# Kernel optimization log

Measured on AMD Instinct MI355X. Metric: run time of the kernel, lower is better.

The kernel has to match this reference:

```python
import jax, jax.numpy as jnp
import numpy as np

N = 1_000_000          # total nodes across the batch of graphs
B = 4096               # number of graphs
EMB = 64               # embed_dim * heads = 32 * 2
FUSED = 3 * EMB        # 192


def _gelu(x):
    # torch nn.GELU default = exact (erf) form
    return jax.nn.gelu(x, approximate=False)


def setup_inputs() -> dict:
    key = jax.random.key(0)
    ks = jax.random.split(key, 30)
    s = 0.02
    inp = {
        "x_ped": jax.random.normal(ks[0], (N, 2), jnp.float32),
        "x_hazard": jax.random.normal(ks[1], (N, 3), jnp.float32),
        "x_infra": jax.random.normal(ks[2], (N, 3), jnp.float32),
        "batch": jnp.sort(jax.random.randint(ks[3], (N,), 0, B)),
        "num_graphs": B,
        # _MLPBranch params: Linear(d, 64) -> GELU -> Linear(64, 64)
        "ped_W1": jax.random.normal(ks[4], (2, EMB), jnp.float32) * s,
        "ped_b1": jnp.zeros((EMB,), jnp.float32),
        "ped_W2": jax.random.normal(ks[5], (EMB, EMB), jnp.float32) * s,
        "ped_b2": jnp.zeros((EMB,), jnp.float32),
        "haz_W1": jax.random.normal(ks[6], (3, EMB), jnp.float32) * s,
        "haz_b1": jnp.zeros((EMB,), jnp.float32),
        "haz_W2": jax.random.normal(ks[7], (EMB, EMB), jnp.float32) * s,
        "haz_b2": jnp.zeros((EMB,), jnp.float32),
        "inf_W1": jax.random.normal(ks[8], (3, EMB), jnp.float32) * s,
        "inf_b1": jnp.zeros((EMB,), jnp.float32),
        "inf_W2": jax.random.normal(ks[9], (EMB, EMB), jnp.float32) * s,
        "inf_b2": jnp.zeros((EMB,), jnp.float32),
        # dense heads
        "fc1_W": jax.random.normal(ks[10], (FUSED, 256), jnp.float32) * s,
        "fc1_b": jnp.zeros((256,), jnp.float32),
        "fc2_W": jax.random.normal(ks[11], (256, 128), jnp.float32) * s,
        "fc2_b": jnp.zeros((128,), jnp.float32),
        "sh_W": jax.random.normal(ks[12], (128, 1), jnp.float32) * s,
        "sh_b": jnp.zeros((1,), jnp.float32),
        "gd_W": jax.random.normal(ks[13], (128, 1), jnp.float32) * s,
        "gd_b": jnp.zeros((1,), jnp.float32),
        # critic: 192 -> 128 -> 64 -> 1 with GELU between
        "c1_W": jax.random.normal(ks[14], (FUSED, 128), jnp.float32) * s,
        "c1_b": jnp.zeros((128,), jnp.float32),
        "c2_W": jax.random.normal(ks[15], (128, 64), jnp.float32) * s,
        "c2_b": jnp.zeros((64,), jnp.float32),
        "c3_W": jax.random.normal(ks[16], (64, 1), jnp.float32) * s,
        "c3_b": jnp.zeros((1,), jnp.float32),
    }
    return inp


def _branch(x, W1, b1, W2, b2):
    # _MLPBranch: Linear -> GELU -> Linear
    return _gelu(x @ W1 + b1) @ W2 + b2


def reference(x_ped, x_hazard, x_infra, batch, num_graphs,
              ped_W1, ped_b1, ped_W2, ped_b2,
              haz_W1, haz_b1, haz_W2, haz_b2,
              inf_W1, inf_b1, inf_W2, inf_b2,
              fc1_W, fc1_b, fc2_W, fc2_b,
              sh_W, sh_b, gd_W, gd_b,
              c1_W, c1_b, c2_W, c2_b, c3_W, c3_b):
    ped_emb = _gelu(_branch(x_ped, ped_W1, ped_b1, ped_W2, ped_b2))
    haz_emb = _gelu(_branch(x_hazard, haz_W1, haz_b1, haz_W2, haz_b2))
    inf_emb = _gelu(_branch(x_infra, inf_W1, inf_b1, inf_W2, inf_b2))
    node_feat = jnp.concatenate([ped_emb, haz_emb, inf_emb], axis=-1)  # (N, 192)

    # per-graph masked mean pooling -> fused segment mean (empty graphs -> zeros)
    seg_sum = jax.ops.segment_sum(node_feat, batch, num_segments=num_graphs)  # (B, 192)
    counts = jax.ops.segment_sum(jnp.ones((node_feat.shape[0],), node_feat.dtype),
                                 batch, num_segments=num_graphs)
    graph_embed = seg_sum / jnp.maximum(counts, 1.0)[:, None]

    dense = _gelu(graph_embed @ fc1_W + fc1_b)
    dense = _gelu(dense @ fc2_W + fc2_b)
    shelter_logits = dense @ sh_W + sh_b
    guidance_logits = dense @ gd_W + gd_b

    v = _gelu(graph_embed @ c1_W + c1_b)
    v = _gelu(v @ c2_W + c2_b)
    value = (v @ c3_W + c3_b).squeeze(-1)
    return shelter_logits, guidance_logits, value
```

## Files before the change

kernel.cpp:

```cpp
#include <hip/hip_runtime.h>
#include <hip/hip_bf16.h>
#include <math.h>

#define EMB 64
#define NFEAT 192

typedef __attribute__((ext_vector_type(8))) short bf16x8;
typedef __attribute__((ext_vector_type(4))) float f32x4;

__device__ __forceinline__ float gelu_n(float x) {
    float y = x * x;
    float G = fmaf(y, fmaf(y, 9.97355701e-3f, -6.64903800e-2f), 3.98942280e-1f);
    return fmaf(0.5f, x, y * G);
}
__device__ __forceinline__ float gelu_head(float x) {
    float y = x * x;
    float G = fmaf(y, fmaf(y, fmaf(y, fmaf(y, 1.15434688e-4f, -1.18732821e-3f),
                                   9.97355701e-3f), -6.64903800e-2f), 3.98942280e-1f);
    float r = fmaf(0.5f, x, y * G);
    if (__builtin_expect(__any(y > 0.25f), 0))
        r = 0.5f * x * (1.0f + erff(x * 0.70710678118654752f));
    return r;
}

__device__ __forceinline__ unsigned short f32_bf16(float f) {
    unsigned u = __float_as_uint(f);
    u = (u + 0x7FFFu + ((u >> 16) & 1u)) >> 16;
    return (unsigned short)u;
}
__device__ __forceinline__ float bf16_f32(unsigned short h) {
    return __uint_as_float(((unsigned)h) << 16);
}

__global__ __launch_bounds__(256) void prep_pack(
    const float* __restrict__ pW2, const float* __restrict__ hW2,
    const float* __restrict__ iW2,
    unsigned short* __restrict__ whi, unsigned short* __restrict__ wlo,
    float4* __restrict__ zbase, int nzero4)
{
    int t = blockIdx.x * blockDim.x + threadIdx.x;
    if (t < nzero4) {
        float4 z = {0.f, 0.f, 0.f, 0.f};
        zbase[t] = z;
    }
    if (t >= 3 * 4096) return;
    int br = t >> 12, r = t & 4095;
    int k = r >> 6, j = r & 63;
    const float* src = br == 0 ? pW2 : (br == 1 ? hW2 : iW2);
    float w = src[k * 64 + j];
    unsigned short hi = f32_bf16(w);
    unsigned short lo = f32_bf16(w - bf16_f32(hi));
    int ks = k >> 5, lgrp = (k >> 3) & 3, i = k & 7;
    int nt = j >> 4, col = j & 15;
    int f = (ks * 4 + nt) * 64 + lgrp * 16 + col;
    whi[br * 4096 + f * 8 + i] = hi;
    wlo[br * 4096 + f * 8 + i] = lo;
}

template <int D>
__device__ __forceinline__ void do_branch(
    const float* __restrict__ xsrc, int n0,
    const float* __restrict__ W1, const float* __restrict__ b1,
    const float* __restrict__ b2,
    const unsigned short* __restrict__ whi, const unsigned short* __restrict__ wlo,
    int lane, int g, int g0, int g63, bool uniform,
    float* __restrict__ seg, float* __restrict__ seg_lane, int boff)
{
    const int lg = lane >> 4, lc = lane & 15;

    float xs[4][3];
#pragma unroll
    for (int m = 0; m < 4; m++) {
        int nm = n0 + m * 16 + lc;
        if (D == 2) {
            float2 t = ((const float2*)xsrc)[nm];
            xs[m][0] = t.x; xs[m][1] = t.y; xs[m][2] = 0.f;
        } else {
            xs[m][0] = xsrc[3 * nm + 0];
            xs[m][1] = xsrc[3 * nm + 1];
            xs[m][2] = xsrc[3 * nm + 2];
        }
    }

    const float* __restrict__ W1p = W1 + lg * 8;
    const float* __restrict__ b1p = b1 + lg * 8;
    const float* __restrict__ b2p = b2 + lc;
    const char*  __restrict__ WHp = (const char*)whi + lane * 16;
    const char*  __restrict__ WLp = (const char*)wlo + lane * 16;

    union AF { bf16x8 v; unsigned u[4]; };
    AF af[4][2];
#pragma unroll
    for (int ks = 0; ks < 2; ks++) {
        float w1r[D][8];
#pragma unroll
        for (int d = 0; d < D; d++) {
            float4 a = *(const float4*)(W1p + ks * 32 + d * EMB);
            float4 b = *(const float4*)(W1p + ks * 32 + d * EMB + 4);
            w1r[d][0] = a.x; w1r[d][1] = a.y; w1r[d][2] = a.z; w1r[d][3] = a.w;
            w1r[d][4] = b.x; w1r[d][5] = b.y; w1r[d][6] = b.z; w1r[d][7] = b.w;
        }
        float4 c0 = *(const float4*)(b1p + ks * 32);
        float4 c1 = *(const float4*)(b1p + ks * 32 + 4);
        float b1r[8] = {c0.x, c0.y, c0.z, c0.w, c1.x, c1.y, c1.z, c1.w};
#pragma unroll
        for (int m = 0; m < 4; m++) {
            float h[8];
#pragma unroll
            for (int i = 0; i < 8; i++) {
                float z = b1r[i];
#pragma unroll
                for (int d = 0; d < D; d++) z = fmaf(xs[m][d], w1r[d][i], z);
                h[i] = gelu_n(z);
            }
#pragma unroll
            for (int j = 0; j < 4; j++)
                asm("v_cvt_pk_bf16_f32 %0, %1, %2"
                    : "=v"(af[m][ks].u[j]) : "v"(h[2 * j]), "v"(h[2 * j + 1]));
        }
    }

    int bn[4][4];
    if (__builtin_expect(!uniform, 0)) {
#pragma unroll
        for (int m = 0; m < 4; m++)
#pragma unroll
            for (int r = 0; r < 4; r++)
                bn[m][r] = __shfl(g, m * 16 + lg * 4 + r, 64);
    }

    float mine = 0.f;
#pragma unroll
    for (int nt = 0; nt < 4; nt++) {
        bf16x8 bh0 = *(const bf16x8*)(WHp + nt * 1024);
        bf16x8 bl0 = *(const bf16x8*)(WLp + nt * 1024);
        bf16x8 bh1 = *(const bf16x8*)(WHp + (4 + nt) * 1024);
        bf16x8 bl1 = *(const bf16x8*)(WLp + (4 + nt) * 1024);
        float bv = b2p[nt * 16];
        f32x4 a[4];
#pragma unroll
        for (int m = 0; m < 4; m++) { f32x4 t = {bv, bv, bv, bv}; a[m] = t; }
#pragma unroll
        for (int m = 0; m < 4; m++)
            a[m] = __builtin_amdgcn_mfma_f32_16x16x32_bf16(af[m][0].v, bh0, a[m], 0, 0, 0);
#pragma unroll
        for (int m = 0; m < 4; m++)
            a[m] = __builtin_amdgcn_mfma_f32_16x16x32_bf16(af[m][0].v, bl0, a[m], 0, 0, 0);
#pragma unroll
        for (int m = 0; m < 4; m++)
            a[m] = __builtin_amdgcn_mfma_f32_16x16x32_bf16(af[m][1].v, bh1, a[m], 0, 0, 0);
#pragma unroll
        for (int m = 0; m < 4; m++)
            a[m] = __builtin_amdgcn_mfma_f32_16x16x32_bf16(af[m][1].v, bl1, a[m], 0, 0, 0);

        if (uniform) {
            float s = 0.f;
#pragma unroll
            for (int m = 0; m < 4; m++)
#pragma unroll
                for (int r = 0; r < 4; r++) s += gelu_n(a[m][r]);
            s += __shfl_xor(s, 16, 64);
            s += __shfl_xor(s, 32, 64);
            if (lg == nt) mine = s;
        } else {
            float ge[4][4];
#pragma unroll
            for (int m = 0; m < 4; m++)
#pragma unroll
                for (int r = 0; r < 4; r++) ge[m][r] = gelu_n(a[m][r]);
            for (int gv = g0; gv <= g63; ++gv) {
                float s = 0.f;
#pragma unroll
                for (int m = 0; m < 4; m++)
#pragma unroll
                    for (int r = 0; r < 4; r++)
                        s += (bn[m][r] == gv) ? ge[m][r] : 0.f;
                s += __shfl_xor(s, 16, 64);
                s += __shfl_xor(s, 32, 64);
                if (lg == nt)
                    atomicAdd(&seg[(size_t)gv * NFEAT + boff + lane], s);
            }
        }
    }
    if (uniform)
        atomicAdd(seg_lane + boff, mine);
}

__global__ __launch_bounds__(256, 4) void node_kernel(
    const float* __restrict__ x_ped, const float* __restrict__ x_haz,
    const float* __restrict__ x_inf, const int* __restrict__ batch,
    const float* __restrict__ ped_W1, const float* __restrict__ ped_b1, const float* __restrict__ ped_b2,
    const float* __restrict__ haz_W1, const float* __restrict__ haz_b1, const float* __restrict__ haz_b2,
    const float* __restrict__ inf_W1, const float* __restrict__ inf_b1, const float* __restrict__ inf_b2,
    const unsigned short* __restrict__ w2hi, const unsigned short* __restrict__ w2lo,
    float* __restrict__ seg, float* __restrict__ counts, int N)
{
    int n0 = ((blockIdx.x * blockDim.x + threadIdx.x) >> 6) << 6;
    if (n0 >= N) return;
    int lane = threadIdx.x & 63;
    int g = batch[n0 + lane];
    int g0 = __shfl(g, 0, 64);
    int g63 = __shfl(g, 63, 64);
    bool uniform = (g0 == g63);

    if (uniform) {
        if (lane == 0) atomicAdd(&counts[g0], 64.0f);
    } else {
        for (int gv = g0; gv <= g63; ++gv) {
            unsigned long long bal = __ballot(g == gv);
            if (lane == 0 && bal) atomicAdd(&counts[gv], (float)__popcll(bal));
        }
    }

    float* seg_lane = seg + (size_t)g0 * NFEAT + lane;

    do_branch<2>(x_ped, n0, ped_W1, ped_b1, ped_b2,
                 w2hi + 0 * 4096, w2lo + 0 * 4096, lane, g, g0, g63, uniform,
                 seg, seg_lane, 0);
    do_branch<3>(x_haz, n0, haz_W1, haz_b1, haz_b2,
                 w2hi + 1 * 4096, w2lo + 1 * 4096, lane, g, g0, g63, uniform,
                 seg, seg_lane, 64);
    do_branch<3>(x_inf, n0, inf_W1, inf_b1, inf_b2,
                 w2hi + 2 * 4096, w2lo + 2 * 4096, lane, g, g0, g63, uniform,
                 seg, seg_lane, 128);
}

__global__ __launch_bounds__(512) void head_kernel(
    const float* __restrict__ seg, const float* __restrict__ counts,
    const float* __restrict__ fc1_W, const float* __restrict__ fc1_b,
    const float* __restrict__ fc2_W, const float* __restrict__ fc2_b,
    const float* __restrict__ sh_W,  const float* __restrict__ sh_b,
    const float* __restrict__ gd_W,  const float* __restrict__ gd_b,
    const float* __restrict__ c1_W,  const float* __restrict__ c1_b,
    const float* __restrict__ c2_W,  const float* __restrict__ c2_b,
    const float* __restrict__ c3_W,  const float* __restrict__ c3_b,
    float* __restrict__ out_sh, float* __restrict__ out_gd, float* __restrict__ out_val,
    int B)
{
    __shared__ float s_emb[16][NFEAT];
    __shared__ float s_a1[16][256];
    __shared__ float s_a2[16][128];
    __shared__ float s_a3[16][128];

    const int wave = threadIdx.x >> 6;
    const int lane = threadIdx.x & 63;
    const int g0 = blockIdx.x * 16 + wave * 2;
    const int ws = wave * 2;
    if (g0 >= B) return;
    const int nq = (B - g0 >= 2) ? 2 : (B - g0);

    for (int q = 0; q < nq; q++) {
        float inv = 1.0f / fmaxf(counts[g0 + q], 1.0f);
#pragma unroll
        for (int r = 0; r < 3; r++)
            s_emb[ws + q][r * 64 + lane] =
                seg[(size_t)(g0 + q) * NFEAT + r * 64 + lane] * inv;
    }

    {
        float4 bb = ((const float4*)fc1_b)[lane];
        float acc[2][4];
#pragma unroll
        for (int q = 0; q < 2; q++) {
            acc[q][0] = bb.x; acc[q][1] = bb.y; acc[q][2] = bb.z; acc[q][3] = bb.w;
        }
        for (int k = 0; k < NFEAT; k++) {
            float4 w = ((const float4*)(fc1_W + k * 256))[lane];
#pragma unroll
            for (int q = 0; q < 2; q++) {
                float e = s_emb[ws + q][k];
                acc[q][0] = fmaf(e, w.x, acc[q][0]);
                acc[q][1] = fmaf(e, w.y, acc[q][1]);
                acc[q][2] = fmaf(e, w.z, acc[q][2]);
                acc[q][3] = fmaf(e, w.w, acc[q][3]);
            }
        }
#pragma unroll
        for (int q = 0; q < 2; q++)
#pragma unroll
            for (int r = 0; r < 4; r++)
                s_a1[ws + q][lane * 4 + r] = gelu_head(acc[q][r]);
    }

    {
        float2 bb = ((const float2*)fc2_b)[lane];
        float acc[2][2];
#pragma unroll
        for (int q = 0; q < 2; q++) { acc[q][0] = bb.x; acc[q][1] = bb.y; }
        for (int k = 0; k < 256; k++) {
            float2 w = ((const float2*)(fc2_W + k * 128))[lane];
#pragma unroll
            for (int q = 0; q < 2; q++) {
                float e = s_a1[ws + q][k];
                acc[q][0] = fmaf(e, w.x, acc[q][0]);
                acc[q][1] = fmaf(e, w.y, acc[q][1]);
            }
        }
#pragma unroll
        for (int q = 0; q < 2; q++) {
            s_a2[ws + q][lane * 2 + 0] = gelu_head(acc[q][0]);
            s_a2[ws + q][lane * 2 + 1] = gelu_head(acc[q][1]);
        }
    }

    {
        float w0 = sh_W[lane], w1 = sh_W[64 + lane];
        float v0 = gd_W[lane], v1 = gd_W[64 + lane];
        float shp[2], gdp[2];
#pragma unroll
        for (int q = 0; q < 2; q++) {
            float a0 = s_a2[ws + q][lane], a1 = s_a2[ws + q][64 + lane];
            shp[q] = fmaf(a0, w0, a1 * w1);
            gdp[q] = fmaf(a0, v0, a1 * v1);
        }
#pragma unroll
        for (int d = 1; d < 64; d <<= 1)
#pragma unroll
            for (int q = 0; q < 2; q++) {
                shp[q] += __shfl_xor(shp[q], d, 64);
                gdp[q] += __shfl_xor(gdp[q], d, 64);
            }
        if (lane == 0) {
            for (int q = 0; q < nq; q++) {
                out_sh[g0 + q] = shp[q] + sh_b[0];
                out_gd[g0 + q] = gdp[q] + gd_b[0];
            }
        }
    }

    {
        float2 bb = ((const float2*)c1_b)[lane];
        float acc[2][2];
#pragma unroll
        for (int q = 0; q < 2; q++) { acc[q][0] = bb.x; acc[q][1] = bb.y; }
        for (int k = 0; k < NFEAT; k++) {
            float2 w = ((const float2*)(c1_W + k * 128))[lane];
#pragma unroll
            for (int q = 0; q < 2; q++) {
                float e = s_emb[ws + q][k];
                acc[q][0] = fmaf(e, w.x, acc[q][0]);
                acc[q][1] = fmaf(e, w.y, acc[q][1]);
            }
        }
#pragma unroll
        for (int q = 0; q < 2; q++) {
            s_a3[ws + q][lane * 2 + 0] = gelu_head(acc[q][0]);
            s_a3[ws + q][lane * 2 + 1] = gelu_head(acc[q][1]);
        }
    }

    {
        float bb = c2_b[lane];
        float acc[2] = {bb, bb};
        for (int k = 0; k < 128; k++) {
            float w = c2_W[k * 64 + lane];
#pragma unroll
            for (int q = 0; q < 2; q++)
                acc[q] = fmaf(s_a3[ws + q][k], w, acc[q]);
        }
        float cw = c3_W[lane];
        float v[2];
#pragma unroll
        for (int q = 0; q < 2; q++) v[q] = gelu_head(acc[q]) * cw;
#pragma unroll
        for (int d = 1; d < 64; d <<= 1)
#pragma unroll
            for (int q = 0; q < 2; q++) v[q] += __shfl_xor(v[q], d, 64);
        if (lane == 0)
            for (int q = 0; q < nq; q++) out_val[g0 + q] = v[q] + c3_b[0];
    }
}

extern "C" void kernel_launch(void* const* d_in, const int* in_sizes, int n_in,
                              void* d_out, int out_size, void* d_ws, size_t ws_size,
                              hipStream_t stream)
{
    const float* x_ped  = (const float*)d_in[0];
    const float* x_haz  = (const float*)d_in[1];
    const float* x_inf  = (const float*)d_in[2];
    const int*   batch  = (const int*)d_in[3];
    const float* ped_W1 = (const float*)d_in[5];
    const float* ped_b1 = (const float*)d_in[6];
    const float* ped_W2 = (const float*)d_in[7];
    const float* ped_b2 = (const float*)d_in[8];
    const float* haz_W1 = (const float*)d_in[9];
    const float* haz_b1 = (const float*)d_in[10];
    const float* haz_W2 = (const float*)d_in[11];
    const float* haz_b2 = (const float*)d_in[12];
    const float* inf_W1 = (const float*)d_in[13];
    const float* inf_b1 = (const float*)d_in[14];
    const float* inf_W2 = (const float*)d_in[15];
    const float* inf_b2 = (const float*)d_in[16];
    const float* fc1_W  = (const float*)d_in[17];
    const float* fc1_b  = (const float*)d_in[18];
    const float* fc2_W  = (const float*)d_in[19];
    const float* fc2_b  = (const float*)d_in[20];
    const float* sh_W   = (const float*)d_in[21];
    const float* sh_b   = (const float*)d_in[22];
    const float* gd_W   = (const float*)d_in[23];
    const float* gd_b   = (const float*)d_in[24];
    const float* c1_W   = (const float*)d_in[25];
    const float* c1_b   = (const float*)d_in[26];
    const float* c2_W   = (const float*)d_in[27];
    const float* c2_b   = (const float*)d_in[28];
    const float* c3_W   = (const float*)d_in[29];
    const float* c3_b   = (const float*)d_in[30];

    int N = in_sizes[3];
    int B = out_size / 3;

    float* seg    = (float*)d_ws;
    float* counts = seg + (size_t)B * NFEAT;
    size_t off = (((size_t)B * (NFEAT + 1) * 4) + 255) & ~(size_t)255;
    unsigned short* w2hi = (unsigned short*)((char*)d_ws + off);
    unsigned short* w2lo = w2hi + 3 * 4096;

    int nzero4 = (B * (NFEAT + 1)) / 4;
    int prep_thr = nzero4 > 3 * 4096 ? nzero4 : 3 * 4096;
    prep_pack<<<(prep_thr + 255) / 256, 256, 0, stream>>>(
        ped_W2, haz_W2, inf_W2, w2hi, w2lo, (float4*)d_ws, nzero4);

    int nblocks = (N + 255) / 256;
    node_kernel<<<nblocks, 256, 0, stream>>>(
        x_ped, x_haz, x_inf, batch,
        ped_W1, ped_b1, ped_b2,
        haz_W1, haz_b1, haz_b2,
        inf_W1, inf_b1, inf_b2,
        w2hi, w2lo, seg, counts, N);

    float* out_sh  = (float*)d_out;
    float* out_gd  = out_sh + B;
    float* out_val = out_gd + B;
    head_kernel<<<(B + 15) / 16, 512, 0, stream>>>(
        seg, counts,
        fc1_W, fc1_b, fc2_W, fc2_b,
        sh_W, sh_b, gd_W, gd_b,
        c1_W, c1_b, c2_W, c2_b, c3_W, c3_b,
        out_sh, out_gd, out_val, B);
}
```

Measured before the change: 288.1 us.

## Fuse node and head kernels using a last-blocks completion ticket

Merges the node embedding/pooling kernel and the dense head kernel into one launch. Each block takes a ticket from a global counter after its node work, and the last headb blocks spin until every block has finished before running the head MLPs, with 4 graphs per wave instead of 2. This removes one kernel launch and the gap between the two kernels. In exchange, occupancy drops because the launch bounds fall from 4 to 3 blocks, the added LDS lowers residency further, and the head stage now runs on only 256 blocks of 4 waves, which reduces its parallelism.

Measured after the change: 354.8 us. +23.1%, slower.

```diff
diff --git a/kernel.cpp b/kernel.cpp
--- a/kernel.cpp
+++ b/kernel.cpp
@@ -4,6 +4,8 @@
 
 #define EMB 64
 #define NFEAT 192
+#define HEADB 256
+#define HEADG 16
 
 typedef __attribute__((ext_vector_type(8))) short bf16x8;
 typedef __attribute__((ext_vector_type(4))) float f32x4;
@@ -186,47 +188,14 @@
         atomicAdd(seg_lane + boff, mine);
 }
 
-__global__ __launch_bounds__(256, 4) void node_kernel(
+__global__ __launch_bounds__(256, 3) void fused_kernel(
     const float* __restrict__ x_ped, const float* __restrict__ x_haz,
     const float* __restrict__ x_inf, const int* __restrict__ batch,
     const float* __restrict__ ped_W1, const float* __restrict__ ped_b1, const float* __restrict__ ped_b2,
     const float* __restrict__ haz_W1, const float* __restrict__ haz_b1, const float* __restrict__ haz_b2,
     const float* __restrict__ inf_W1, const float* __restrict__ inf_b1, const float* __restrict__ inf_b2,
     const unsigned short* __restrict__ w2hi, const unsigned short* __restrict__ w2lo,
-    float* __restrict__ seg, float* __restrict__ counts, int N)
-{
-    int n0 = ((blockIdx.x * blockDim.x + threadIdx.x) >> 6) << 6;
-    if (n0 >= N) return;
-    int lane = threadIdx.x & 63;
-    int g = batch[n0 + lane];
-    int g0 = __shfl(g, 0, 64);
-    int g63 = __shfl(g, 63, 64);
-    bool uniform = (g0 == g63);
-
-    if (uniform) {
-        if (lane == 0) atomicAdd(&counts[g0], 64.0f);
-    } else {
-        for (int gv = g0; gv <= g63; ++gv) {
-            unsigned long long bal = __ballot(g == gv);
-            if (lane == 0 && bal) atomicAdd(&counts[gv], (float)__popcll(bal));
-        }
-    }
-
-    float* seg_lane = seg + (size_t)g0 * NFEAT + lane;
-
-    do_branch<2>(x_ped, n0, ped_W1, ped_b1, ped_b2,
-                 w2hi + 0 * 4096, w2lo + 0 * 4096, lane, g, g0, g63, uniform,
-                 seg, seg_lane, 0);
-    do_branch<3>(x_haz, n0, haz_W1, haz_b1, haz_b2,
-                 w2hi + 1 * 4096, w2lo + 1 * 4096, lane, g, g0, g63, uniform,
-                 seg, seg_lane, 64);
-    do_branch<3>(x_inf, n0, inf_W1, inf_b1, inf_b2,
-                 w2hi + 2 * 4096, w2lo + 2 * 4096, lane, g, g0, g63, uniform,
-                 seg, seg_lane, 128);
-}
-
-__global__ __launch_bounds__(512) void head_kernel(
-    const float* __restrict__ seg, const float* __restrict__ counts,
+    float* __restrict__ seg, float* __restrict__ counts, int* __restrict__ done_ctr,
     const float* __restrict__ fc1_W, const float* __restrict__ fc1_b,
     const float* __restrict__ fc2_W, const float* __restrict__ fc2_b,
     const float* __restrict__ sh_W,  const float* __restrict__ sh_b,
@@ -235,39 +204,89 @@
     const float* __restrict__ c2_W,  const float* __restrict__ c2_b,
     const float* __restrict__ c3_W,  const float* __restrict__ c3_b,
     float* __restrict__ out_sh, float* __restrict__ out_gd, float* __restrict__ out_val,
-    int B)
+    int N, int B, int nblocks, int headb)
 {
-    __shared__ float s_emb[16][NFEAT];
-    __shared__ float s_a1[16][256];
-    __shared__ float s_a2[16][128];
-    __shared__ float s_a3[16][128];
-
-    const int wave = threadIdx.x >> 6;
+    __shared__ int sticket;
+    __shared__ float s_emb[HEADG][NFEAT];
+    __shared__ float s_a1[HEADG][256];
+    __shared__ float s_a2[HEADG][128];
+    __shared__ float s_a3[HEADG][128];
+
     const int lane = threadIdx.x & 63;
-    const int g0 = blockIdx.x * 16 + wave * 2;
-    const int ws = wave * 2;
-    if (g0 >= B) return;
-    const int nq = (B - g0 >= 2) ? 2 : (B - g0);
+    const int wv = threadIdx.x >> 6;
+
+    {
+        int n0 = (blockIdx.x * 4 + wv) << 6;
+        if (n0 < N) {
+            int g = batch[n0 + lane];
+            int g0 = __shfl(g, 0, 64);
+            int g63 = __shfl(g, 63, 64);
+            bool uniform = (g0 == g63);
+
+            if (uniform) {
+                if (lane == 0) atomicAdd(&counts[g0], 64.0f);
+            } else {
+                for (int gv = g0; gv <= g63; ++gv) {
+                    unsigned long long bal = __ballot(g == gv);
+                    if (lane == 0 && bal) atomicAdd(&counts[gv], (float)__popcll(bal));
+                }
+            }
+
+            float* seg_lane = seg + (size_t)g0 * NFEAT + lane;
+
+            do_branch<2>(x_ped, n0, ped_W1, ped_b1, ped_b2,
+                         w2hi + 0 * 4096, w2lo + 0 * 4096, lane, g, g0, g63, uniform,
+                         seg, seg_lane, 0);
+            do_branch<3>(x_haz, n0, haz_W1, haz_b1, haz_b2,
+                         w2hi + 1 * 4096, w2lo + 1 * 4096, lane, g, g0, g63, uniform,
+                         seg, seg_lane, 64);
+            do_branch<3>(x_inf, n0, inf_W1, inf_b1, inf_b2,
+                         w2hi + 2 * 4096, w2lo + 2 * 4096, lane, g, g0, g63, uniform,
+                         seg, seg_lane, 128);
+        }
+    }
+
+    __syncthreads();
+    if (threadIdx.x == 0) sticket = atomicAdd(done_ctr, 1);
+    __syncthreads();
+    int hb = sticket - (nblocks - headb);
+    if (hb < 0) return;
+
+    if (threadIdx.x == 0) {
+        while (__hip_atomic_load(done_ctr, __ATOMIC_ACQUIRE, __HIP_MEMORY_SCOPE_AGENT) < nblocks)
+            __builtin_amdgcn_s_sleep(8);
+    }
+    __syncthreads();
+
+    const int gbase = hb * HEADG + wv * 4;
+    const int ws = wv * 4;
+    int nq = B - gbase;
+    if (nq <= 0) return;
+    if (nq > 4) nq = 4;
 
     for (int q = 0; q < nq; q++) {
-        float inv = 1.0f / fmaxf(counts[g0 + q], 1.0f);
-#pragma unroll
-        for (int r = 0; r < 3; r++)
-            s_emb[ws + q][r * 64 + lane] =
-                seg[(size_t)(g0 + q) * NFEAT + r * 64 + lane] * inv;
+        int gg = gbase + q;
+        float cnt = __hip_atomic_load(&counts[gg], __ATOMIC_RELAXED, __HIP_MEMORY_SCOPE_AGENT);
+        float inv = 1.0f / fmaxf(cnt, 1.0f);
+#pragma unroll
+        for (int r = 0; r < 3; r++) {
+            float v = __hip_atomic_load(&seg[(size_t)gg * NFEAT + r * 64 + lane],
+                                        __ATOMIC_RELAXED, __HIP_MEMORY_SCOPE_AGENT);
+            s_emb[ws + q][r * 64 + lane] = v * inv;
+        }
     }
 
     {
         float4 bb = ((const float4*)fc1_b)[lane];
-        float acc[2][4];
-#pragma unroll
-        for (int q = 0; q < 2; q++) {
+        float acc[4][4];
+#pragma unroll
+        for (int q = 0; q < 4; q++) {
             acc[q][0] = bb.x; acc[q][1] = bb.y; acc[q][2] = bb.z; acc[q][3] = bb.w;
         }
         for (int k = 0; k < NFEAT; k++) {
             float4 w = ((const float4*)(fc1_W + k * 256))[lane];
 #pragma unroll
-            for (int q = 0; q < 2; q++) {
+            for (int q = 0; q < 4; q++) {
                 float e = s_emb[ws + q][k];
                 acc[q][0] = fmaf(e, w.x, acc[q][0]);
                 acc[q][1] = fmaf(e, w.y, acc[q][1]);
@@ -276,7 +295,7 @@
             }
         }
 #pragma unroll
-        for (int q = 0; q < 2; q++)
+        for (int q = 0; q < 4; q++)
 #pragma unroll
             for (int r = 0; r < 4; r++)
                 s_a1[ws + q][lane * 4 + r] = gelu_head(acc[q][r]);
@@ -284,20 +303,20 @@
 
     {
         float2 bb = ((const float2*)fc2_b)[lane];
-        float acc[2][2];
-#pragma unroll
-        for (int q = 0; q < 2; q++) { acc[q][0] = bb.x; acc[q][1] = bb.y; }
+        float acc[4][2];
+#pragma unroll
+        for (int q = 0; q < 4; q++) { acc[q][0] = bb.x; acc[q][1] = bb.y; }
         for (int k = 0; k < 256; k++) {
             float2 w = ((const float2*)(fc2_W + k * 128))[lane];
 #pragma unroll
-            for (int q = 0; q < 2; q++) {
+            for (int q = 0; q < 4; q++) {
                 float e = s_a1[ws + q][k];
                 acc[q][0] = fmaf(e, w.x, acc[q][0]);
                 acc[q][1] = fmaf(e, w.y, acc[q][1]);
             }
         }
 #pragma unroll
-        for (int q = 0; q < 2; q++) {
+        for (int q = 0; q < 4; q++) {
             s_a2[ws + q][lane * 2 + 0] = gelu_head(acc[q][0]);
             s_a2[ws + q][lane * 2 + 1] = gelu_head(acc[q][1]);
         }
@@ -306,9 +325,9 @@
     {
         float w0 = sh_W[lane], w1 = sh_W[64 + lane];
         float v0 = gd_W[lane], v1 = gd_W[64 + lane];
-        float shp[2], gdp[2];
-#pragma unroll
-        for (int q = 0; q < 2; q++) {
+        float shp[4], gdp[4];
+#pragma unroll
+        for (int q = 0; q < 4; q++) {
             float a0 = s_a2[ws + q][lane], a1 = s_a2[ws + q][64 + lane];
             shp[q] = fmaf(a0, w0, a1 * w1);
             gdp[q] = fmaf(a0, v0, a1 * v1);
@@ -316,34 +335,34 @@
 #pragma unroll
         for (int d = 1; d < 64; d <<= 1)
 #pragma unroll
-            for (int q = 0; q < 2; q++) {
+            for (int q = 0; q < 4; q++) {
                 shp[q] += __shfl_xor(shp[q], d, 64);
                 gdp[q] += __shfl_xor(gdp[q], d, 64);
             }
         if (lane == 0) {
             for (int q = 0; q < nq; q++) {
-                out_sh[g0 + q] = shp[q] + sh_b[0];
-                out_gd[g0 + q] = gdp[q] + gd_b[0];
+                out_sh[gbase + q] = shp[q] + sh_b[0];
+                out_gd[gbase + q] = gdp[q] + gd_b[0];
             }
         }
     }
 
     {
         float2 bb = ((const float2*)c1_b)[lane];
-        float acc[2][2];
-#pragma unroll
-        for (int q = 0; q < 2; q++) { acc[q][0] = bb.x; acc[q][1] = bb.y; }
+        float acc[4][2];
+#pragma unroll
+        for (int q = 0; q < 4; q++) { acc[q][0] = bb.x; acc[q][1] = bb.y; }
         for (int k = 0; k < NFEAT; k++) {
             float2 w = ((const float2*)(c1_W + k * 128))[lane];
 #pragma unroll
-            for (int q = 0; q < 2; q++) {
+            for (int q = 0; q < 4; q++) {
                 float e = s_emb[ws + q][k];
                 acc[q][0] = fmaf(e, w.x, acc[q][0]);
                 acc[q][1] = fmaf(e, w.y, acc[q][1]);
             }
         }
 #pragma unroll
-        for (int q = 0; q < 2; q++) {
+        for (int q = 0; q < 4; q++) {
             s_a3[ws + q][lane * 2 + 0] = gelu_head(acc[q][0]);
             s_a3[ws + q][lane * 2 + 1] = gelu_head(acc[q][1]);
         }
@@ -351,23 +370,23 @@
 
     {
         float bb = c2_b[lane];
-        float acc[2] = {bb, bb};
+        float acc[4] = {bb, bb, bb, bb};
         for (int k = 0; k < 128; k++) {
             float w = c2_W[k * 64 + lane];
 #pragma unroll
-            for (int q = 0; q < 2; q++)
+            for (int q = 0; q < 4; q++)
                 acc[q] = fmaf(s_a3[ws + q][k], w, acc[q]);
         }
         float cw = c3_W[lane];
-        float v[2];
-#pragma unroll
-        for (int q = 0; q < 2; q++) v[q] = gelu_head(acc[q]) * cw;
+        float v[4];
+#pragma unroll
+        for (int q = 0; q < 4; q++) v[q] = gelu_head(acc[q]) * cw;
 #pragma unroll
         for (int d = 1; d < 64; d <<= 1)
 #pragma unroll
-            for (int q = 0; q < 2; q++) v[q] += __shfl_xor(v[q], d, 64);
+            for (int q = 0; q < 4; q++) v[q] += __shfl_xor(v[q], d, 64);
         if (lane == 0)
-            for (int q = 0; q < nq; q++) out_val[g0 + q] = v[q] + c3_b[0];
+            for (int q = 0; q < nq; q++) out_val[gbase + q] = v[q] + c3_b[0];
     }
 }
 
@@ -411,30 +430,34 @@
 
     float* seg    = (float*)d_ws;
     float* counts = seg + (size_t)B * NFEAT;
-    size_t off = (((size_t)B * (NFEAT + 1) * 4) + 255) & ~(size_t)255;
+    int*   done_ctr = (int*)(counts + B);
+    size_t zbytes = ((size_t)B * (NFEAT + 1) + 4) * sizeof(float);
+    size_t off = (zbytes + 255) & ~(size_t)255;
     unsigned short* w2hi = (unsigned short*)((char*)d_ws + off);
     unsigned short* w2lo = w2hi + 3 * 4096;
 
-    int nzero4 = (B * (NFEAT + 1)) / 4;
+    int nzero4 = (int)(zbytes / 16);
     int prep_thr = nzero4 > 3 * 4096 ? nzero4 : 3 * 4096;
     prep_pack<<<(prep_thr + 255) / 256, 256, 0, stream>>>(
         ped_W2, haz_W2, inf_W2, w2hi, w2lo, (float4*)d_ws, nzero4);
 
-    int nblocks = (N + 255) / 256;
-    node_kernel<<<nblocks, 256, 0, stream>>>(
+    int nwaves = (N + 63) / 64;
+    int nblocks = (nwaves + 3) / 4;
+    int headb = (B + HEADG - 1) / HEADG;
+
+    float* out_sh  = (float*)d_out;
+    float* out_gd  = out_sh + B;
+    float* out_val = out_gd + B;
+
+    fused_kernel<<<nblocks, 256, 0, stream>>>(
         x_ped, x_haz, x_inf, batch,
         ped_W1, ped_b1, ped_b2,
         haz_W1, haz_b1, haz_b2,
         inf_W1, inf_b1, inf_b2,
-        w2hi, w2lo, seg, counts, N);
-
-    float* out_sh  = (float*)d_out;
-    float* out_gd  = out_sh + B;
-    float* out_val = out_gd + B;
-    head_kernel<<<(B + 15) / 16, 512, 0, stream>>>(
-        seg, counts,
+        w2hi, w2lo, seg, counts, done_ctr,
         fc1_W, fc1_b, fc2_W, fc2_b,
         sh_W, sh_b, gd_W, gd_b,
         c1_W, c1_b, c2_W, c2_b, c3_W, c3_b,
-        out_sh, out_gd, out_val, B);
-}
+        out_sh, out_gd, out_val,
+        N, B, nblocks, headb);
+}
```

## Restructure head kernel to share weight loads across eight graphs per block

Applied to the files above, without the earlier changes.

Rewrites the head MLP kernel so that each block handles eight graphs together. Each thread owns one output column and accumulates all eight graphs, so every weight element loaded from global memory is reused eight times instead of twice. Activations are stored transposed in shared memory ([k][graph]) and read as float4. Some layers split the K dimension across half-waves and reduce with shuffles. Block size drops to 256 with block-wide syncs between layers, which adds barrier overhead and produces fewer blocks (512) to spread across CUs.

Result: faster. 271.4 us (-5.8%).

```diff
diff --git a/kernel.cpp b/kernel.cpp
--- a/kernel.cpp
+++ b/kernel.cpp
@@ -4,6 +4,7 @@
 
 #define EMB 64
 #define NFEAT 192
+#define GQ 8
 
 typedef __attribute__((ext_vector_type(8))) short bf16x8;
 typedef __attribute__((ext_vector_type(4))) float f32x4;
@@ -225,7 +226,7 @@
                  seg, seg_lane, 128);
 }
 
-__global__ __launch_bounds__(512) void head_kernel(
+__global__ __launch_bounds__(256, 2) void head_kernel(
     const float* __restrict__ seg, const float* __restrict__ counts,
     const float* __restrict__ fc1_W, const float* __restrict__ fc1_b,
     const float* __restrict__ fc2_W, const float* __restrict__ fc2_b,
@@ -237,137 +238,243 @@
     float* __restrict__ out_sh, float* __restrict__ out_gd, float* __restrict__ out_val,
     int B)
 {
-    __shared__ float s_emb[16][NFEAT];
-    __shared__ float s_a1[16][256];
-    __shared__ float s_a2[16][128];
-    __shared__ float s_a3[16][128];
-
-    const int wave = threadIdx.x >> 6;
-    const int lane = threadIdx.x & 63;
-    const int g0 = blockIdx.x * 16 + wave * 2;
-    const int ws = wave * 2;
+    __shared__ float s_emb[NFEAT][GQ];
+    __shared__ float s_a1[256][GQ];
+    __shared__ float s_a2[128][GQ];
+    __shared__ float s_a3[128][GQ];
+    __shared__ float s_c2[64][GQ];
+
+    const int tid = threadIdx.x;
+    const int wave = tid >> 6;
+    const int lane = tid & 63;
+    const int g0 = blockIdx.x * GQ;
     if (g0 >= B) return;
-    const int nq = (B - g0 >= 2) ? 2 : (B - g0);
-
-    for (int q = 0; q < nq; q++) {
-        float inv = 1.0f / fmaxf(counts[g0 + q], 1.0f);
-#pragma unroll
-        for (int r = 0; r < 3; r++)
-            s_emb[ws + q][r * 64 + lane] =
-                seg[(size_t)(g0 + q) * NFEAT + r * 64 + lane] * inv;
-    }
+    const int nq = (B - g0 >= GQ) ? GQ : (B - g0);
+
+    if (tid < NFEAT) {
+#pragma unroll
+        for (int q = 0; q < GQ; q++) {
+            float v = 0.f;
+            if (q < nq) {
+                float inv = 1.0f / fmaxf(counts[g0 + q], 1.0f);
+                v = seg[(size_t)(g0 + q) * NFEAT + tid] * inv;
+            }
+            s_emb[tid][q] = v;
+        }
+    }
+    __syncthreads();
 
     {
-        float4 bb = ((const float4*)fc1_b)[lane];
-        float acc[2][4];
-#pragma unroll
-        for (int q = 0; q < 2; q++) {
-            acc[q][0] = bb.x; acc[q][1] = bb.y; acc[q][2] = bb.z; acc[q][3] = bb.w;
-        }
-        for (int k = 0; k < NFEAT; k++) {
-            float4 w = ((const float4*)(fc1_W + k * 256))[lane];
-#pragma unroll
-            for (int q = 0; q < 2; q++) {
-                float e = s_emb[ws + q][k];
-                acc[q][0] = fmaf(e, w.x, acc[q][0]);
-                acc[q][1] = fmaf(e, w.y, acc[q][1]);
-                acc[q][2] = fmaf(e, w.z, acc[q][2]);
-                acc[q][3] = fmaf(e, w.w, acc[q][3]);
+        int j = wave * 64 + lane;
+        const float* __restrict__ Wp = fc1_W + j;
+        float bb = fc1_b[j];
+        float acc[GQ];
+#pragma unroll
+        for (int q = 0; q < GQ; q++) acc[q] = bb;
+        for (int k0 = 0; k0 < NFEAT; k0 += 4) {
+            float w0 = Wp[(k0 + 0) * 256], w1 = Wp[(k0 + 1) * 256];
+            float w2 = Wp[(k0 + 2) * 256], w3 = Wp[(k0 + 3) * 256];
+            float4 ea0 = *(const float4*)&s_emb[k0 + 0][0], eb0 = *(const float4*)&s_emb[k0 + 0][4];
+            float4 ea1 = *(const float4*)&s_emb[k0 + 1][0], eb1 = *(const float4*)&s_emb[k0 + 1][4];
+            float4 ea2 = *(const float4*)&s_emb[k0 + 2][0], eb2 = *(const float4*)&s_emb[k0 + 2][4];
+            float4 ea3 = *(const float4*)&s_emb[k0 + 3][0], eb3 = *(const float4*)&s_emb[k0 + 3][4];
+            acc[0] = fmaf(ea0.x, w0, acc[0]); acc[1] = fmaf(ea0.y, w0, acc[1]);
+            acc[2] = fmaf(ea0.z, w0, acc[2]); acc[3] = fmaf(ea0.w, w0, acc[3]);
+            acc[4] = fmaf(eb0.x, w0, acc[4]); acc[5] = fmaf(eb0.y, w0, acc[5]);
+            acc[6] = fmaf(eb0.z, w0, acc[6]); acc[7] = fmaf(eb0.w, w0, acc[7]);
+            acc[0] = fmaf(ea1.x, w1, acc[0]); acc[1] = fmaf(ea1.y, w1, acc[1]);
+            acc[2] = fmaf(ea1.z, w1, acc[2]); acc[3] = fmaf(ea1.w, w1, acc[3]);
+            acc[4] = fmaf(eb1.x, w1, acc[4]); acc[5] = fmaf(eb1.y, w1, acc[5]);
+            acc[6] = fmaf(eb1.z, w1, acc[6]); acc[7] = fmaf(eb1.w, w1, acc[7]);
+            acc[0] = fmaf(ea2.x, w2, acc[0]); acc[1] = fmaf(ea2.y, w2, acc[1]);
+            acc[2] = fmaf(ea2.z, w2, acc[2]); acc[3] = fmaf(ea2.w, w2, acc[3]);
+            acc[4] = fmaf(eb2.x, w2, acc[4]); acc[5] = fmaf(eb2.y, w2, acc[5]);
+            acc[6] = fmaf(eb2.z, w2, acc[6]); acc[7] = fmaf(eb2.w, w2, acc[7]);
+            acc[0] = fmaf(ea3.x, w3, acc[0]); acc[1] = fmaf(ea3.y, w3, acc[1]);
+            acc[2] = fmaf(ea3.z, w3, acc[2]); acc[3] = fmaf(ea3.w, w3, acc[3]);
+            acc[4] = fmaf(eb3.x, w3, acc[4]); acc[5] = fmaf(eb3.y, w3, acc[5]);
+            acc[6] = fmaf(eb3.z, w3, acc[6]); acc[7] = fmaf(eb3.w, w3, acc[7]);
+        }
+        float4 lo, hi;
+        lo.x = gelu_head(acc[0]); lo.y = gelu_head(acc[1]);
+        lo.z = gelu_head(acc[2]); lo.w = gelu_head(acc[3]);
+        hi.x = gelu_head(acc[4]); hi.y = gelu_head(acc[5]);
+        hi.z = gelu_head(acc[6]); hi.w = gelu_head(acc[7]);
+        *(float4*)&s_a1[j][0] = lo;
+        *(float4*)&s_a1[j][4] = hi;
+    }
+    __syncthreads();
+
+    {
+        int j = wave * 32 + (lane & 31);
+        int kh = lane >> 5;
+        const float* __restrict__ Wp = fc2_W + j;
+        float bb = fc2_b[j];
+        float acc[GQ];
+#pragma unroll
+        for (int q = 0; q < GQ; q++) acc[q] = (kh == 0) ? bb : 0.f;
+        int kbeg = kh * 128;
+        for (int k0 = kbeg; k0 < kbeg + 128; k0 += 4) {
+            float w0 = Wp[(k0 + 0) * 128], w1 = Wp[(k0 + 1) * 128];
+            float w2 = Wp[(k0 + 2) * 128], w3 = Wp[(k0 + 3) * 128];
+            float4 ea0 = *(const float4*)&s_a1[k0 + 0][0], eb0 = *(const float4*)&s_a1[k0 + 0][4];
+            float4 ea1 = *(const float4*)&s_a1[k0 + 1][0], eb1 = *(const float4*)&s_a1[k0 + 1][4];
+            float4 ea2 = *(const float4*)&s_a1[k0 + 2][0], eb2 = *(const float4*)&s_a1[k0 + 2][4];
+            float4 ea3 = *(const float4*)&s_a1[k0 + 3][0], eb3 = *(const float4*)&s_a1[k0 + 3][4];
+            acc[0] = fmaf(ea0.x, w0, acc[0]); acc[1] = fmaf(ea0.y, w0, acc[1]);
+            acc[2] = fmaf(ea0.z, w0, acc[2]); acc[3] = fmaf(ea0.w, w0, acc[3]);
+            acc[4] = fmaf(eb0.x, w0, acc[4]); acc[5] = fmaf(eb0.y, w0, acc[5]);
+            acc[6] = fmaf(eb0.z, w0, acc[6]); acc[7] = fmaf(eb0.w, w0, acc[7]);
+            acc[0] = fmaf(ea1.x, w1, acc[0]); acc[1] = fmaf(ea1.y, w1, acc[1]);
+            acc[2] = fmaf(ea1.z, w1, acc[2]); acc[3] = fmaf(ea1.w, w1, acc[3]);
+            acc[4] = fmaf(eb1.x, w1, acc[4]); acc[5] = fmaf(eb1.y, w1, acc[5]);
+            acc[6] = fmaf(eb1.z, w1, acc[6]); acc[7] = fmaf(eb1.w, w1, acc[7]);
+            acc[0] = fmaf(ea2.x, w2, acc[0]); acc[1] = fmaf(ea2.y, w2, acc[1]);
+            acc[2] = fmaf(ea2.z, w2, acc[2]); acc[3] = fmaf(ea2.w, w2, acc[3]);
+            acc[4] = fmaf(eb2.x, w2, acc[4]); acc[5] = fmaf(eb2.y, w2, acc[5]);
+            acc[6] = fmaf(eb2.z, w2, acc[6]); acc[7] = fmaf(eb2.w, w2, acc[7]);
+            acc[0] = fmaf(ea3.x, w3, acc[0]); acc[1] = fmaf(ea3.y, w3, acc[1]);
+            acc[2] = fmaf(ea3.z, w3, acc[2]); acc[3] = fmaf(ea3.w, w3, acc[3]);
+            acc[4] = fmaf(eb3.x, w3, acc[4]); acc[5] = fmaf(eb3.y, w3, acc[5]);
+            acc[6] = fmaf(eb3.z, w3, acc[6]); acc[7] = fmaf(eb3.w, w3, acc[7]);
+        }
+#pragma unroll
+        for (int q = 0; q < GQ; q++) acc[q] += __shfl_xor(acc[q], 32, 64);
+        if (kh == 0) {
+            float4 lo, hi;
+            lo.x = gelu_head(acc[0]); lo.y = gelu_head(acc[1]);
+            lo.z = gelu_head(acc[2]); lo.w = gelu_head(acc[3]);
+            hi.x = gelu_head(acc[4]); hi.y = gelu_head(acc[5]);
+            hi.z = gelu_head(acc[6]); hi.w = gelu_head(acc[7]);
+            *(float4*)&s_a2[j][0] = lo;
+            *(float4*)&s_a2[j][4] = hi;
+        }
+    }
+    __syncthreads();
+
+    {
+        int j = wave * 32 + (lane & 31);
+        int kh = lane >> 5;
+        const float* __restrict__ Wp = c1_W + j;
+        float bb = c1_b[j];
+        float acc[GQ];
+#pragma unroll
+        for (int q = 0; q < GQ; q++) acc[q] = (kh == 0) ? bb : 0.f;
+        int kbeg = kh * 96;
+        for (int k0 = kbeg; k0 < kbeg + 96; k0 += 4) {
+            float w0 = Wp[(k0 + 0) * 128], w1 = Wp[(k0 + 1) * 128];
+            float w2 = Wp[(k0 + 2) * 128], w3 = Wp[(k0 + 3) * 128];
+            float4 ea0 = *(const float4*)&s_emb[k0 + 0][0], eb0 = *(const float4*)&s_emb[k0 + 0][4];
+            float4 ea1 = *(const float4*)&s_emb[k0 + 1][0], eb1 = *(const float4*)&s_emb[k0 + 1][4];
+            float4 ea2 = *(const float4*)&s_emb[k0 + 2][0], eb2 = *(const float4*)&s_emb[k0 + 2][4];
+            float4 ea3 = *(const float4*)&s_emb[k0 + 3][0], eb3 = *(const float4*)&s_emb[k0 + 3][4];
+            acc[0] = fmaf(ea0.x, w0, acc[0]); acc[1] = fmaf(ea0.y, w0, acc[1]);
+            acc[2] = fmaf(ea0.z, w0, acc[2]); acc[3] = fmaf(ea0.w, w0, acc[3]);
+            acc[4] = fmaf(eb0.x, w0, acc[4]); acc[5] = fmaf(eb0.y, w0, acc[5]);
+            acc[6] = fmaf(eb0.z, w0, acc[6]); acc[7] = fmaf(eb0.w, w0, acc[7]);
+            acc[0] = fmaf(ea1.x, w1, acc[0]); acc[1] = fmaf(ea1.y, w1, acc[1]);
+            acc[2] = fmaf(ea1.z, w1, acc[2]); acc[3] = fmaf(ea1.w, w1, acc[3]);
+            acc[4] = fmaf(eb1.x, w1, acc[4]); acc[5] = fmaf(eb1.y, w1, acc[5]);
+            acc[6] = fmaf(eb1.z, w1, acc[6]); acc[7] = fmaf(eb1.w, w1, acc[7]);
+            acc[0] = fmaf(ea2.x, w2, acc[0]); acc[1] = fmaf(ea2.y, w2, acc[1]);
+            acc[2] = fmaf(ea2.z, w2, acc[2]); acc[3] = fmaf(ea2.w, w2, acc[3]);
+            acc[4] = fmaf(eb2.x, w2, acc[4]); acc[5] = fmaf(eb2.y, w2, acc[5]);
+            acc[6] = fmaf(eb2.z, w2, acc[6]); acc[7] = fmaf(eb2.w, w2, acc[7]);
+            acc[0] = fmaf(ea3.x, w3, acc[0]); acc[1] = fmaf(ea3.y, w3, acc[1]);
+            acc[2] = fmaf(ea3.z, w3, acc[2]); acc[3] = fmaf(ea3.w, w3, acc[3]);
+            acc[4] = fmaf(eb3.x, w3, acc[4]); acc[5] = fmaf(eb3.y, w3, acc[5]);
+            acc[6] = fmaf(eb3.z, w3, acc[6]); acc[7] = fmaf(eb3.w, w3, acc[7]);
+        }
+#pragma unroll
+        for (int q = 0; q < GQ; q++) acc[q] += __shfl_xor(acc[q], 32, 64);
+        if (kh == 0) {
+            float4 lo, hi;
+            lo.x = gelu_head(acc[0]); lo.y = gelu_head(acc[1]);
+            lo.z = gelu_head(acc[2]); lo.w = gelu_head(acc[3]);
+            hi.x = gelu_head(acc[4]); hi.y = gelu_head(acc[5]);
+            hi.z = gelu_head(acc[6]); hi.w = gelu_head(acc[7]);
+            *(float4*)&s_a3[j][0] = lo;
+            *(float4*)&s_a3[j][4] = hi;
+        }
+    }
+    __syncthreads();
+
+    {
+        int j = wave * 16 + (lane & 15);
+        int kp = lane >> 4;
+        const float* __restrict__ Wp = c2_W + j;
+        float bb = c2_b[j];
+        float acc[GQ];
+#pragma unroll
+        for (int q = 0; q < GQ; q++) acc[q] = (kp == 0) ? bb : 0.f;
+        int kbeg = kp * 32;
+        for (int k0 = kbeg; k0 < kbeg + 32; k0 += 4) {
+            float w0 = Wp[(k0 + 0) * 64], w1 = Wp[(k0 + 1) * 64];
+            float w2 = Wp[(k0 + 2) * 64], w3 = Wp[(k0 + 3) * 64];
+            float4 ea0 = *(const float4*)&s_a3[k0 + 0][0], eb0 = *(const float4*)&s_a3[k0 + 0][4];
+            float4 ea1 = *(const float4*)&s_a3[k0 + 1][0], eb1 = *(const float4*)&s_a3[k0 + 1][4];
+            float4 ea2 = *(const float4*)&s_a3[k0 + 2][0], eb2 = *(const float4*)&s_a3[k0 + 2][4];
+            float4 ea3 = *(const float4*)&s_a3[k0 + 3][0], eb3 = *(const float4*)&s_a3[k0 + 3][4];
+            acc[0] = fmaf(ea0.x, w0, acc[0]); acc[1] = fmaf(ea0.y, w0, acc[1]);
+            acc[2] = fmaf(ea0.z, w0, acc[2]); acc[3] = fmaf(ea0.w, w0, acc[3]);
+            acc[4] = fmaf(eb0.x, w0, acc[4]); acc[5] = fmaf(eb0.y, w0, acc[5]);
+            acc[6] = fmaf(eb0.z, w0, acc[6]); acc[7] = fmaf(eb0.w, w0, acc[7]);
+            acc[0] = fmaf(ea1.x, w1, acc[0]); acc[1] = fmaf(ea1.y, w1, acc[1]);
+            acc[2] = fmaf(ea1.z, w1, acc[2]); acc[3] = fmaf(ea1.w, w1, acc[3]);
+            acc[4] = fmaf(eb1.x, w1, acc[4]); acc[5] = fmaf(eb1.y, w1, acc[5]);
+            acc[6] = fmaf(eb1.z, w1, acc[6]); acc[7] = fmaf(eb1.w, w1, acc[7]);
+            acc[0] = fmaf(ea2.x, w2, acc[0]); acc[1] = fmaf(ea2.y, w2, acc[1]);
+            acc[2] = fmaf(ea2.z, w2, acc[2]); acc[3] = fmaf(ea2.w, w2, acc[3]);
+            acc[4] = fmaf(eb2.x, w2, acc[4]); acc[5] = fmaf(eb2.y, w2, acc[5]);
+            acc[6] = fmaf(eb2.z, w2, acc[6]); acc[7] = fmaf(eb2.w, w2, acc[7]);
+            acc[0] = fmaf(ea3.x, w3, acc[0]); acc[1] = fmaf(ea3.y, w3, acc[1]);
+            acc[2] = fmaf(ea3.z, w3, acc[2]); acc[3] = fmaf(ea3.w, w3, acc[3]);
+            acc[4] = fmaf(eb3.x, w3, acc[4]); acc[5] = fmaf(eb3.y, w3, acc[5]);
+            acc[6] = fmaf(eb3.z, w3, acc[6]); acc[7] = fmaf(eb3.w, w3, acc[7]);
+        }
+#pragma unroll
+        for (int q = 0; q < GQ; q++) {
+            acc[q] += __shfl_xor(acc[q], 16, 64);
+            acc[q] += __shfl_xor(acc[q], 32, 64);
+        }
+        if (kp == 0) {
+            float4 lo, hi;
+            lo.x = gelu_head(acc[0]); lo.y = gelu_head(acc[1]);
+            lo.z = gelu_head(acc[2]); lo.w = gelu_head(acc[3]);
+            hi.x = gelu_head(acc[4]); hi.y = gelu_head(acc[5]);
+            hi.z = gelu_head(acc[6]); hi.w = gelu_head(acc[7]);
+            *(float4*)&s_c2[j][0] = lo;
+            *(float4*)&s_c2[j][4] = hi;
+        }
+    }
+    __syncthreads();
+
+    if (wave < 3) {
+        int q = lane >> 3;
+        int c = lane & 7;
+        float s = 0.f;
+        if (wave < 2) {
+            const float* wv = (wave == 0) ? sh_W : gd_W;
+#pragma unroll
+            for (int kk = 0; kk < 16; kk++) {
+                int k = c * 16 + kk;
+                s = fmaf(s_a2[k][q], wv[k], s);
             }
-        }
-#pragma unroll
-        for (int q = 0; q < 2; q++)
-#pragma unroll
-            for (int r = 0; r < 4; r++)
-                s_a1[ws + q][lane * 4 + r] = gelu_head(acc[q][r]);
-    }
-
-    {
-        float2 bb = ((const float2*)fc2_b)[lane];
-        float acc[2][2];
-#pragma unroll
-        for (int q = 0; q < 2; q++) { acc[q][0] = bb.x; acc[q][1] = bb.y; }
-        for (int k = 0; k < 256; k++) {
-            float2 w = ((const float2*)(fc2_W + k * 128))[lane];
-#pragma unroll
-            for (int q = 0; q < 2; q++) {
-                float e = s_a1[ws + q][k];
-                acc[q][0] = fmaf(e, w.x, acc[q][0]);
-                acc[q][1] = fmaf(e, w.y, acc[q][1]);
+        } else {
+#pragma unroll
+            for (int kk = 0; kk < 8; kk++) {
+                int k = c * 8 + kk;
+                s = fmaf(s_c2[k][q], c3_W[k], s);
             }
         }
-#pragma unroll
-        for (int q = 0; q < 2; q++) {
-            s_a2[ws + q][lane * 2 + 0] = gelu_head(acc[q][0]);
-            s_a2[ws + q][lane * 2 + 1] = gelu_head(acc[q][1]);
-        }
-    }
-
-    {
-        float w0 = sh_W[lane], w1 = sh_W[64 + lane];
-        float v0 = gd_W[lane], v1 = gd_W[64 + lane];
-        float shp[2], gdp[2];
-#pragma unroll
-        for (int q = 0; q < 2; q++) {
-            float a0 = s_a2[ws + q][lane], a1 = s_a2[ws + q][64 + lane];
-            shp[q] = fmaf(a0, w0, a1 * w1);
-            gdp[q] = fmaf(a0, v0, a1 * v1);
-        }
-#pragma unroll
-        for (int d = 1; d < 64; d <<= 1)
-#pragma unroll
-            for (int q = 0; q < 2; q++) {
-                shp[q] += __shfl_xor(shp[q], d, 64);
-                gdp[q] += __shfl_xor(gdp[q], d, 64);
-            }
-        if (lane == 0) {
-            for (int q = 0; q < nq; q++) {
-                out_sh[g0 + q] = shp[q] + sh_b[0];
-                out_gd[g0 + q] = gdp[q] + gd_b[0];
-            }
-        }
-    }
-
-    {
-        float2 bb = ((const float2*)c1_b)[lane];
-        float acc[2][2];
-#pragma unroll
-        for (int q = 0; q < 2; q++) { acc[q][0] = bb.x; acc[q][1] = bb.y; }
-        for (int k = 0; k < NFEAT; k++) {
-            float2 w = ((const float2*)(c1_W + k * 128))[lane];
-#pragma unroll
-            for (int q = 0; q < 2; q++) {
-                float e = s_emb[ws + q][k];
-                acc[q][0] = fmaf(e, w.x, acc[q][0]);
-                acc[q][1] = fmaf(e, w.y, acc[q][1]);
-            }
-        }
-#pragma unroll
-        for (int q = 0; q < 2; q++) {
-            s_a3[ws + q][lane * 2 + 0] = gelu_head(acc[q][0]);
-            s_a3[ws + q][lane * 2 + 1] = gelu_head(acc[q][1]);
-        }
-    }
-
-    {
-        float bb = c2_b[lane];
-        float acc[2] = {bb, bb};
-        for (int k = 0; k < 128; k++) {
-            float w = c2_W[k * 64 + lane];
-#pragma unroll
-            for (int q = 0; q < 2; q++)
-                acc[q] = fmaf(s_a3[ws + q][k], w, acc[q]);
-        }
-        float cw = c3_W[lane];
-        float v[2];
-#pragma unroll
-        for (int q = 0; q < 2; q++) v[q] = gelu_head(acc[q]) * cw;
-#pragma unroll
-        for (int d = 1; d < 64; d <<= 1)
-#pragma unroll
-            for (int q = 0; q < 2; q++) v[q] += __shfl_xor(v[q], d, 64);
-        if (lane == 0)
-            for (int q = 0; q < nq; q++) out_val[g0 + q] = v[q] + c3_b[0];
+        s += __shfl_xor(s, 1, 64);
+        s += __shfl_xor(s, 2, 64);
+        s += __shfl_xor(s, 4, 64);
+        if (c == 0 && q < nq) {
+            if (wave == 0)      out_sh[g0 + q] = s + sh_b[0];
+            else if (wave == 1) out_gd[g0 + q] = s + gd_b[0];
+            else                out_val[g0 + q] = s + c3_b[0];
+        }
     }
 }
 
@@ -431,7 +538,7 @@
     float* out_sh  = (float*)d_out;
     float* out_gd  = out_sh + B;
     float* out_val = out_gd + B;
-    head_kernel<<<(B + 15) / 16, 512, 0, stream>>>(
+    head_kernel<<<(B + GQ - 1) / GQ, 256, 0, stream>>>(
         seg, counts,
         fc1_W, fc1_b, fc2_W, fc2_b,
         sh_W, sh_b, gd_W, gd_b,
```
